# Kernel tuning notes

Hardware: AMD Instinct MI355X
Metric: run time of the kernel (lower is better)

The kernel has to match this reference:

```python
import jax, jax.numpy as jnp
import numpy as np

CONFIDENCE = 0.1
EPS = 1e-3  # keras BatchNormalization default epsilon
B, H, W, C = 4, 64, 64, 256


def setup_inputs() -> dict:
    key = jax.random.key(0)
    ks = jax.random.split(key, 6)
    return {
        "x": jax.random.normal(ks[0], (B, H, W, C), jnp.float32),
        "ca_gamma": jnp.ones((C,), jnp.float32),
        "ca_beta": jnp.zeros((C,), jnp.float32),
        "ca_mean": jnp.zeros((C,), jnp.float32),
        "ca_var": jnp.ones((C,), jnp.float32),
        "wq": jax.random.normal(ks[1], (C, C), jnp.float32) * 0.05,
        "wk": jax.random.normal(ks[2], (C, C), jnp.float32) * 0.05,
        "wv": jax.random.normal(ks[3], (C, C), jnp.float32) * 0.05,
        "wp": jax.random.normal(ks[4], (C, C), jnp.float32) * 0.05,
        "bn_gamma": jnp.ones((C,), jnp.float32),
        "bn_beta": jnp.zeros((C,), jnp.float32),
        "bn_mean": jnp.zeros((C,), jnp.float32),
        "bn_var": jnp.ones((C,), jnp.float32),
        "w_qkv": jax.random.normal(ks[5], (C, 3), jnp.float32) * 0.05,
    }


def _bn(x, g, b, m, v):
    # keras BatchNormalization, inference mode
    return (x - m) * jax.lax.rsqrt(v + EPS) * g + b


def reference(x, ca_gamma, ca_beta, ca_mean, ca_var, wq, wk, wv, wp,
              bn_gamma, bn_beta, bn_mean, bn_var, w_qkv):
    b, h, w, c = x.shape
    # ---- ChannelAttention (TRACER Channel_Tracer; dropout = identity at inference) ----
    gap = x.mean(axis=(1, 2))                         # [B, C] global average pool
    gn = _bn(gap, ca_gamma, ca_beta, ca_mean, ca_var)  # [B, C]
    q = gn @ wq                                        # 1x1 conv on 1x1 map == matmul
    k = gn @ wk
    v = gn @ wv
    logits = q[:, :, None] * k[:, None, :]             # [B, C, C], head_dim = 1
    score = jax.nn.softmax(logits, axis=-1)
    att = jnp.einsum('bij,bj->bi', score, v)           # [B, C]
    cmask = jax.nn.sigmoid(att @ wp)                   # [B, C] channel mask (alpha)
    ca_out = x * cmask[:, None, None, :] + x           # residual channel re-weighting
    # ---- UnionAttention spatial part ----
    co = _bn(ca_out, bn_gamma, bn_beta, bn_mean, bn_var)
    thr = jnp.percentile(cmask, CONFIDENCE * 100.0, axis=-1,
                         keepdims=True, method='linear')  # [B, 1]
    pmask = jnp.where(cmask > thr, cmask, 0.0)          # percentile masking
    co = co * pmask[:, None, None, :]
    qkv = jnp.einsum('bhwc,cf->bhwf', co, w_qkv)        # [B, H, W, 3] fused q/k/v 1x1 conv
    n = h * w
    qs = qkv[..., 0].reshape(b, n)                      # [B, N], head_dim = 1
    ks_ = qkv[..., 1].reshape(b, n)
    vs = qkv[..., 2].reshape(b, n)
    sl = qs[:, :, None] * ks_[:, None, :]               # [B, N, N] scores (outer product)
    sw = jax.nn.softmax(sl, axis=-1)
    sa = jnp.einsum('bij,bj->bi', sw, vs)               # [B, N]
    return qkv[..., 2:3] + sa.reshape(b, h, w, 1)       # v + attention, [B, H, W, 1]
```

## Files before the change

kernel.cpp:

```cpp
#include <hip/hip_runtime.h>

#define EPS 1e-3f

#define OFF_PGAP   0
#define OFF_PART   81920
#define OFF_AW     196608
#define OFF_BIAS   198656
#define OFF_QS     215040
#define OFF_KS     231424
#define OFF_VS     247808

#define L2E 1.4426950408889634f

__device__ __forceinline__ void st_wt2(float* p, float a, float b) {
    union { float f[2]; unsigned long long u; } x; x.f[0] = a; x.f[1] = b;
    __hip_atomic_store((unsigned long long*)p, x.u, __ATOMIC_RELAXED,
                       __HIP_MEMORY_SCOPE_AGENT);
}

__device__ unsigned g_done;

__global__ __launch_bounds__(512) void k_gap(
    const float* __restrict__ x,
    const float* __restrict__ wq, const float* __restrict__ wk,
    const float* __restrict__ wv, const float* __restrict__ wp,
    const float* __restrict__ bng, const float* __restrict__ bnb,
    const float* __restrict__ bnm, const float* __restrict__ bnv,
    const float* __restrict__ cag, const float* __restrict__ cab,
    const float* __restrict__ cam, const float* __restrict__ cav,
    float* __restrict__ pgap)
{
    __shared__ float4 s4[512];
    int blk = blockIdx.x;
    int t = threadIdx.x;
    int lane = t & 63, sub = t >> 6;

    if (t < 256) {
        const float* wmat = (blk < 64) ? wq : (blk < 128) ? wk
                          : (blk < 192) ? wv : wp;
        float4 w4 = *(const float4*)(wmat + (size_t)(blk & 63) * 1024 + 4 * t);
        asm volatile("" :: "v"(w4.x), "v"(w4.y), "v"(w4.z), "v"(w4.w));
    }
    if (blk == 1 && t < 256) {
        float z = bng[t] + bnb[t] + bnm[t] + bnv[t];
        asm volatile("" :: "v"(z));
    }
    if (blk == 2 && t < 256) {
        float z = cag[t] + cab[t] + cam[t] + cav[t];
        asm volatile("" :: "v"(z));
    }

    const float* xp = x + ((size_t)blk * 64 + sub * 8) * 256 + 4 * lane;
    float4 s = make_float4(0.f, 0.f, 0.f, 0.f);
    #pragma unroll
    for (int u = 0; u < 8; ++u) {
        float4 v = *(const float4*)(xp + (size_t)u * 256);
        s.x += v.x; s.y += v.y; s.z += v.z; s.w += v.w;
    }
    s4[sub * 64 + lane] = s;
    __syncthreads();
    if (t < 64) {
        float4 o = s4[t];
        #pragma unroll
        for (int p = 1; p < 8; ++p) {
            float4 v = s4[p * 64 + t];
            o.x += v.x; o.y += v.y; o.z += v.z; o.w += v.w;
        }
        *(float4*)(pgap + blk * 256 + 4 * t) = o;
    }
}

__global__ __launch_bounds__(512) void k_qkvmid(
    const float* __restrict__ pgap,
    const float* __restrict__ cag, const float* __restrict__ cab,
    const float* __restrict__ cam, const float* __restrict__ cav,
    const float* __restrict__ wq, const float* __restrict__ wk,
    const float* __restrict__ wv, const float* __restrict__ wp,
    const float* __restrict__ bng, const float* __restrict__ bnb,
    const float* __restrict__ bnm, const float* __restrict__ bnv,
    const float* __restrict__ wqkv,
    float* __restrict__ part, float* __restrict__ Aw, float* __restrict__ biasW)
{
    __shared__ float smem[4360];
    __shared__ int sBatch;
    int blk = blockIdx.x;
    int m = blk / 32, g = blk % 32;
    int r0 = g * 8;
    int t = threadIdx.x;
    int lane = t & 63, sub = t >> 6;
    const float* W = (m == 0) ? wq : (m == 1) ? wk : wv;

    {
        float* gpart = smem;
        float* gn_s  = smem + 512;
        float* red   = smem + 1536;
        {
            int b = t >> 7, row = (t >> 4) & 7, p4 = t & 15;
            float s = 0.f;
            #pragma unroll
            for (int q = 0; q < 4; ++q)
                s += pgap[(size_t)(b * 64 + p4 * 4 + q) * 256 + r0 + row];
            gpart[b * 128 + row * 16 + p4] = s;
        }
        __syncthreads();
        if (t < 32) {
            int b = t >> 3, row = t & 7;
            float s = 0.f;
            #pragma unroll
            for (int p = 0; p < 16; ++p) s += gpart[b * 128 + row * 16 + p];
            float gv = s * (1.0f / 4096.0f);
            int c = r0 + row;
            float sc = cag[c] * rsqrtf(cav[c] + EPS);
            gn_s[b * 8 + row] = gv * sc + (cab[c] - cam[c] * sc);
        }
        __syncthreads();
        {
            int c = t & 255, h = t >> 8;
            float a0 = 0.f, a1 = 0.f, a2 = 0.f, a3 = 0.f;
            #pragma unroll
            for (int rr = 0; rr < 4; ++rr) {
                int ri = h * 4 + rr;
                float w = W[(size_t)(r0 + ri) * 256 + c];
                a0 = fmaf(gn_s[0 * 8 + ri], w, a0);
                a1 = fmaf(gn_s[1 * 8 + ri], w, a1);
                a2 = fmaf(gn_s[2 * 8 + ri], w, a2);
                a3 = fmaf(gn_s[3 * 8 + ri], w, a3);
            }
            red[(h * 4 + 0) * 256 + c] = a0;
            red[(h * 4 + 1) * 256 + c] = a1;
            red[(h * 4 + 2) * 256 + c] = a2;
            red[(h * 4 + 3) * 256 + c] = a3;
        }
        __syncthreads();
        {
            int b = t >> 7, c0 = (t & 127) * 2;
            float v0 = red[b * 256 + c0]     + red[(4 + b) * 256 + c0];
            float v1 = red[b * 256 + c0 + 1] + red[(4 + b) * 256 + c0 + 1];
            st_wt2(part + (size_t)((m * 32 + g) * 4 + b) * 256 + c0, v0, v1);
        }
    }
    __syncthreads();
    if (t == 0) {
        unsigned v = __hip_atomic_fetch_add(&g_done, 1u, __ATOMIC_ACQ_REL,
                                            __HIP_MEMORY_SCOPE_AGENT);
        unsigned r = v % 96u;
        int batch = (int)r - 92;
        if (batch >= 0) {
            unsigned target = v - r + 96u;
            unsigned tries = 0;
            while (__hip_atomic_load(&g_done, __ATOMIC_RELAXED,
                                     __HIP_MEMORY_SCOPE_AGENT) < target) {
                __builtin_amdgcn_s_sleep(1);
                if (++tries > 8000000u) break;
            }
        }
        sBatch = batch;
    }
    __syncthreads();
    if (sBatch < 0) return;

    {
        int b = sBatch;
        float* sq  = smem;
        float* sk  = smem + 256;
        float* sv  = smem + 512;
        float* att = smem + 768;
        float* cmv = smem + 1024;
        float* Bc  = smem + 1280;
        float* red = smem + 1536;
        float* swq = smem + 3584;
        float* sc2 = smem + 4352;

        if (t < 384) { swq[t] = wqkv[t]; swq[t + 384] = wqkv[t + 384]; }

        if (t < 384) {
            int mm = t >> 7, c0 = (t & 127) * 2;
            float a0 = 0.f, a1 = 0.f;
            #pragma unroll 8
            for (int gg = 0; gg < 32; ++gg) {
                float2 v = *(const float2*)(part +
                              (size_t)((mm * 32 + gg) * 4 + b) * 256 + c0);
                a0 += v.x; a1 += v.y;
            }
            float* dst = (mm == 0) ? sq : (mm == 1) ? sk : sv;
            dst[c0] = a0; dst[c0 + 1] = a1;
        }
        __syncthreads();

        if (t < 64) {
            float mx = -1e30f, mn = 1e30f;
            #pragma unroll
            for (int u = 0; u < 4; ++u) {
                float v = sk[t + u * 64];
                mx = fmaxf(mx, v); mn = fminf(mn, v);
            }
            #pragma unroll
            for (int m2 = 1; m2 < 64; m2 <<= 1) {
                mx = fmaxf(mx, __shfl_xor(mx, m2, 64));
                mn = fminf(mn, __shfl_xor(mn, m2, 64));
            }
            if (t == 0) { sc2[0] = mx; sc2[1] = mn; }
        }
        __syncthreads();

        {
            int c = t & 255, h = t >> 8;
            float a = sq[c];
            float mrow = (a >= 0.f) ? a * sc2[0] : a * sc2[1];
            float a2 = a * L2E, m2 = mrow * L2E;
            const float* skp = sk + h * 128;
            const float* svp = sv + h * 128;
            float den = 0.f, num = 0.f;
            #pragma unroll 4
            for (int j = 0; j < 128; ++j) {
                float e = __builtin_amdgcn_exp2f(fmaf(a2, skp[j], -m2));
                den += e; num = fmaf(e, svp[j], num);
            }
            red[h * 256 + c] = den;
            red[512 + h * 256 + c] = num;
        }
        __syncthreads();
        if (t < 256)
            att[t] = (red[512 + t] + red[768 + t]) / (red[t] + red[256 + t]);
        __syncthreads();

        {
            int rg = sub, c4 = lane * 4;
            float4 ac = make_float4(0.f, 0.f, 0.f, 0.f);
            const float* wpp = wp + (size_t)rg * 32 * 256 + c4;
            #pragma unroll 8
            for (int i = 0; i < 32; ++i) {
                float gv = att[rg * 32 + i];
                float4 w = *(const float4*)(wpp + (size_t)i * 256);
                ac.x = fmaf(gv, w.x, ac.x); ac.y = fmaf(gv, w.y, ac.y);
                ac.z = fmaf(gv, w.z, ac.z); ac.w = fmaf(gv, w.w, ac.w);
            }
            *(float4*)(red + rg * 256 + c4) = ac;
        }
        __syncthreads();
        if (t < 256) {
            float ac = 0.f;
            #pragma unroll
            for (int r = 0; r < 8; ++r) ac += red[r * 256 + t];
            cmv[t] = 1.0f / (1.0f + __expf(-ac));
        }
        __syncthreads();

        if (t < 256) {
            float my = cmv[t];
            int rank = 0;
            for (int j = 0; j < 256; ++j) {
                float o = cmv[j];
                rank += (o < my) ? 1 : ((o == my && j < t) ? 1 : 0);
            }
            if (rank == 25) sc2[2] = my;
            if (rank == 26) sc2[3] = my;
        }
        __syncthreads();
        if (t == 0) sc2[4] = sc2[2] + 0.5f * (sc2[3] - sc2[2]);
        __syncthreads();

        if (t < 256) {
            float s2 = bng[t] * rsqrtf(bnv[t] + EPS);
            float o2 = bnb[t] - bnm[t] * s2;
            float cc = cmv[t];
            float pm = (cc > sc2[4]) ? cc : 0.f;
            Aw[b * 256 + t] = (1.f + cc) * s2 * pm;
            Bc[t] = o2 * pm;
        }
        __syncthreads();
        if (t < 3) {
            float s3 = 0.f;
            for (int ch = 0; ch < 256; ++ch)
                s3 = fmaf(Bc[ch], swq[ch * 3 + t], s3);
            biasW[b * 3 + t] = s3;
        }
    }
}

__global__ __launch_bounds__(256) void k_qkv(
    const float* __restrict__ x, const float* __restrict__ A,
    const float* __restrict__ wqkv, const float* __restrict__ bias,
    float* __restrict__ qs, float* __restrict__ ks, float* __restrict__ vs)
{
    int t = threadIdx.x;
    int lane = t & 63;
    int sl = lane & 31;
    int half = lane >> 5;
    int wid = (blockIdx.x * 256 + t) >> 6;
    union { float4 v4[6]; float f[24]; } W;
    #pragma unroll
    for (int i = 0; i < 6; ++i)
        W.v4[i] = *(const float4*)(wqkv + 24 * sl + 4 * i);
    #pragma unroll
    for (int b = 0; b < 4; ++b) {
        int pix = b * 4096 + wid * 2 + half;
        const float* xp = x + (size_t)pix * 256 + sl * 8;
        float4 xv0 = *(const float4*)(xp);
        float4 xv1 = *(const float4*)(xp + 4);
        float4 a0 = *(const float4*)(A + b * 256 + sl * 8);
        float4 a1 = *(const float4*)(A + b * 256 + sl * 8 + 4);
        float bq = bias[b * 3 + 0];
        float bk = bias[b * 3 + 1];
        float bv = bias[b * 3 + 2];
        float tt0 = xv0.x * a0.x, tt1 = xv0.y * a0.y;
        float tt2 = xv0.z * a0.z, tt3 = xv0.w * a0.w;
        float tt4 = xv1.x * a1.x, tt5 = xv1.y * a1.y;
        float tt6 = xv1.z * a1.z, tt7 = xv1.w * a1.w;
        float q = tt0 * W.f[0] + tt1 * W.f[3] + tt2 * W.f[6] + tt3 * W.f[9]
                + tt4 * W.f[12] + tt5 * W.f[15] + tt6 * W.f[18] + tt7 * W.f[21];
        float k = tt0 * W.f[1] + tt1 * W.f[4] + tt2 * W.f[7] + tt3 * W.f[10]
                + tt4 * W.f[13] + tt5 * W.f[16] + tt6 * W.f[19] + tt7 * W.f[22];
        float v = tt0 * W.f[2] + tt1 * W.f[5] + tt2 * W.f[8] + tt3 * W.f[11]
                + tt4 * W.f[14] + tt5 * W.f[17] + tt6 * W.f[20] + tt7 * W.f[23];
        #pragma unroll
        for (int m2 = 1; m2 < 32; m2 <<= 1) {
            q += __shfl_xor(q, m2, 64);
            k += __shfl_xor(k, m2, 64);
            v += __shfl_xor(v, m2, 64);
        }
        if (sl == 0) {
            qs[pix] = q + bq; ks[pix] = k + bk; vs[pix] = v + bv;
        }
    }
}

__global__ __launch_bounds__(512) void k_attn2(
    const float* __restrict__ qs, const float* __restrict__ ks,
    const float* __restrict__ vs, float* __restrict__ out)
{
    __shared__ float4 skv[2048];
    __shared__ float pden[8][64], pnum[8][64];
    __shared__ float rmax[8], rmin[8];
    int blk = blockIdx.x;
    int b = blk >> 6, ic = blk & 63;
    int t = threadIdx.x;
    int lane = t & 63, sub = t >> 6;
    int base = b * 4096;

    const float4* k4 = (const float4*)(ks + base);
    const float4* v4 = (const float4*)(vs + base);
    float kmx = -1e30f, kmn = 1e30f;
    #pragma unroll
    for (int u = 0; u < 2; ++u) {
        int i = t + u * 512;
        float4 kk = k4[i], vv = v4[i];
        skv[i * 2]     = make_float4(kk.x, vv.x, kk.y, vv.y);
        skv[i * 2 + 1] = make_float4(kk.z, vv.z, kk.w, vv.w);
        kmx = fmaxf(kmx, fmaxf(fmaxf(kk.x, kk.y), fmaxf(kk.z, kk.w)));
        kmn = fminf(kmn, fminf(fminf(kk.x, kk.y), fminf(kk.z, kk.w)));
    }
    #pragma unroll
    for (int m2 = 1; m2 < 64; m2 <<= 1) {
        kmx = fmaxf(kmx, __shfl_xor(kmx, m2, 64));
        kmn = fminf(kmn, __shfl_xor(kmn, m2, 64));
    }
    if (lane == 0) { rmax[sub] = kmx; rmin[sub] = kmn; }
    __syncthreads();
    float mx = rmax[0], mn = rmin[0];
    #pragma unroll
    for (int s = 1; s < 8; ++s) { mx = fmaxf(mx, rmax[s]); mn = fminf(mn, rmin[s]); }

    int row = ic * 64 + lane;
    float a = qs[base + row];
    float mrow = (a >= 0.f) ? a * mx : a * mn;
    float a2 = a * L2E, m2v = mrow * L2E;
    float den0 = 0.f, num0 = 0.f, den1 = 0.f, num1 = 0.f;
    const float4* sp = skv + sub * 256;
    #pragma unroll 4
    for (int j = 0; j < 256; ++j) {
        float4 kv = sp[j];
        float e0 = __builtin_amdgcn_exp2f(fmaf(a2, kv.x, -m2v));
        float e1 = __builtin_amdgcn_exp2f(fmaf(a2, kv.z, -m2v));
        den0 += e0; num0 = fmaf(e0, kv.y, num0);
        den1 += e1; num1 = fmaf(e1, kv.w, num1);
    }
    pden[sub][lane] = den0 + den1;
    pnum[sub][lane] = num0 + num1;
    __syncthreads();
    if (t < 64) {
        float den = 0.f, num = 0.f;
        #pragma unroll
        for (int s = 0; s < 8; ++s) { den += pden[s][t]; num += pnum[s][t]; }
        int r = ic * 64 + t;
        float vrow = (r & 1) ? skv[r >> 1].w : skv[r >> 1].y;
        out[base + r] = vrow + num / den;
    }
}

extern "C" void kernel_launch(void* const* d_in, const int* in_sizes, int n_in,
                              void* d_out, int out_size, void* d_ws, size_t ws_size,
                              hipStream_t stream) {
    const float* x    = (const float*)d_in[0];
    const float* cag  = (const float*)d_in[1];
    const float* cab  = (const float*)d_in[2];
    const float* cam  = (const float*)d_in[3];
    const float* cav  = (const float*)d_in[4];
    const float* wq   = (const float*)d_in[5];
    const float* wk   = (const float*)d_in[6];
    const float* wv   = (const float*)d_in[7];
    const float* wp   = (const float*)d_in[8];
    const float* bng  = (const float*)d_in[9];
    const float* bnb  = (const float*)d_in[10];
    const float* bnm  = (const float*)d_in[11];
    const float* bnv  = (const float*)d_in[12];
    const float* wqkv = (const float*)d_in[13];

    float* ws   = (float*)d_ws;
    float* pgap = ws + OFF_PGAP;
    float* part = ws + OFF_PART;
    float* Aw   = ws + OFF_AW;
    float* bias = ws + OFF_BIAS;
    float* qs   = ws + OFF_QS;
    float* ks   = ws + OFF_KS;
    float* vs   = ws + OFF_VS;

    k_gap<<<dim3(256), dim3(512), 0, stream>>>(x, wq, wk, wv, wp,
                                               bng, bnb, bnm, bnv,
                                               cag, cab, cam, cav, pgap);
    k_qkvmid<<<dim3(96), dim3(512), 0, stream>>>(pgap, cag, cab, cam, cav,
                                                 wq, wk, wv, wp,
                                                 bng, bnb, bnm, bnv, wqkv,
                                                 part, Aw, bias);
    k_qkv<<<dim3(512), dim3(256), 0, stream>>>(x, Aw, wqkv, bias, qs, ks, vs);
    k_attn2<<<dim3(256), dim3(512), 0, stream>>>(qs, ks, vs, (float*)d_out);
}
```

Baseline: 126.8 us.

## Fuse four kernels into two using device-wide atomic grid barriers

```diff
diff --git a/kernel.cpp b/kernel.cpp
--- a/kernel.cpp
+++ b/kernel.cpp
@@ -6,72 +6,26 @@
 #define OFF_PART   81920
 #define OFF_AW     196608
 #define OFF_BIAS   198656
-#define OFF_QS     215040
-#define OFF_KS     231424
+#define OFF_KS     215040
 #define OFF_VS     247808
 
 #define L2E 1.4426950408889634f
 
+__device__ __forceinline__ void st_wt(float* p, float v) {
+    __hip_atomic_store(p, v, __ATOMIC_RELAXED, __HIP_MEMORY_SCOPE_AGENT);
+}
 __device__ __forceinline__ void st_wt2(float* p, float a, float b) {
     union { float f[2]; unsigned long long u; } x; x.f[0] = a; x.f[1] = b;
     __hip_atomic_store((unsigned long long*)p, x.u, __ATOMIC_RELAXED,
                        __HIP_MEMORY_SCOPE_AGENT);
 }
 
+__device__ unsigned g_ctr1;
 __device__ unsigned g_done;
-
-__global__ __launch_bounds__(512) void k_gap(
+__device__ unsigned g_doneB[4 * 32];
+
+__global__ __launch_bounds__(512) void k_gapmid(
     const float* __restrict__ x,
-    const float* __restrict__ wq, const float* __restrict__ wk,
-    const float* __restrict__ wv, const float* __restrict__ wp,
-    const float* __restrict__ bng, const float* __restrict__ bnb,
-    const float* __restrict__ bnm, const float* __restrict__ bnv,
-    const float* __restrict__ cag, const float* __restrict__ cab,
-    const float* __restrict__ cam, const float* __restrict__ cav,
-    float* __restrict__ pgap)
-{
-    __shared__ float4 s4[512];
-    int blk = blockIdx.x;
-    int t = threadIdx.x;
-    int lane = t & 63, sub = t >> 6;
-
-    if (t < 256) {
-        const float* wmat = (blk < 64) ? wq : (blk < 128) ? wk
-                          : (blk < 192) ? wv : wp;
-        float4 w4 = *(const float4*)(wmat + (size_t)(blk & 63) * 1024 + 4 * t);
-        asm volatile("" :: "v"(w4.x), "v"(w4.y), "v"(w4.z), "v"(w4.w));
-    }
-    if (blk == 1 && t < 256) {
-        float z = bng[t] + bnb[t] + bnm[t] + bnv[t];
-        asm volatile("" :: "v"(z));
-    }
-    if (blk == 2 && t < 256) {
-        float z = cag[t] + cab[t] + cam[t] + cav[t];
-        asm volatile("" :: "v"(z));
-    }
-
-    const float* xp = x + ((size_t)blk * 64 + sub * 8) * 256 + 4 * lane;
-    float4 s = make_float4(0.f, 0.f, 0.f, 0.f);
-    #pragma unroll
-    for (int u = 0; u < 8; ++u) {
-        float4 v = *(const float4*)(xp + (size_t)u * 256);
-        s.x += v.x; s.y += v.y; s.z += v.z; s.w += v.w;
-    }
-    s4[sub * 64 + lane] = s;
-    __syncthreads();
-    if (t < 64) {
-        float4 o = s4[t];
-        #pragma unroll
-        for (int p = 1; p < 8; ++p) {
-            float4 v = s4[p * 64 + t];
-            o.x += v.x; o.y += v.y; o.z += v.z; o.w += v.w;
-        }
-        *(float4*)(pgap + blk * 256 + 4 * t) = o;
-    }
-}
-
-__global__ __launch_bounds__(512) void k_qkvmid(
-    const float* __restrict__ pgap,
     const float* __restrict__ cag, const float* __restrict__ cab,
     const float* __restrict__ cam, const float* __restrict__ cav,
     const float* __restrict__ wq, const float* __restrict__ wk,
@@ -79,17 +33,72 @@
     const float* __restrict__ bng, const float* __restrict__ bnb,
     const float* __restrict__ bnm, const float* __restrict__ bnv,
     const float* __restrict__ wqkv,
-    float* __restrict__ part, float* __restrict__ Aw, float* __restrict__ biasW)
+    float* __restrict__ pgap, float* __restrict__ part,
+    float* __restrict__ Aw, float* __restrict__ biasW)
 {
     __shared__ float smem[4360];
     __shared__ int sBatch;
     int blk = blockIdx.x;
+    int t = threadIdx.x;
+    int lane = t & 63, sub = t >> 6;
+
+    {
+        if (t < 256) {
+            const float* wmat = (blk < 64) ? wq : (blk < 128) ? wk
+                              : (blk < 192) ? wv : wp;
+            float4 w4 = *(const float4*)(wmat + (size_t)(blk & 63) * 1024 + 4 * t);
+            asm volatile("" :: "v"(w4.x), "v"(w4.y), "v"(w4.z), "v"(w4.w));
+        }
+        if (blk == 1 && t < 256) {
+            float z = bng[t] + bnb[t] + bnm[t] + bnv[t];
+            asm volatile("" :: "v"(z));
+        }
+        if (blk == 2 && t < 256) {
+            float z = cag[t] + cab[t] + cam[t] + cav[t];
+            asm volatile("" :: "v"(z));
+        }
+        float4* s4 = (float4*)smem;
+        const float* xp = x + ((size_t)blk * 64 + sub * 8) * 256 + 4 * lane;
+        float4 s = make_float4(0.f, 0.f, 0.f, 0.f);
+        #pragma unroll
+        for (int u = 0; u < 8; ++u) {
+            float4 v = *(const float4*)(xp + (size_t)u * 256);
+            s.x += v.x; s.y += v.y; s.z += v.z; s.w += v.w;
+        }
+        s4[sub * 64 + lane] = s;
+        __syncthreads();
+        if (t < 64) {
+            float4 o = s4[t];
+            #pragma unroll
+            for (int p = 1; p < 8; ++p) {
+                float4 v = s4[p * 64 + t];
+                o.x += v.x; o.y += v.y; o.z += v.z; o.w += v.w;
+            }
+            st_wt2(pgap + blk * 256 + 4 * t,     o.x, o.y);
+            st_wt2(pgap + blk * 256 + 4 * t + 2, o.z, o.w);
+        }
+    }
+    __syncthreads();
+
+    if (t == 0) {
+        unsigned v = __hip_atomic_fetch_add(&g_ctr1, 1u, __ATOMIC_ACQ_REL,
+                                            __HIP_MEMORY_SCOPE_AGENT);
+        if (blk < 96) {
+            unsigned target = v - (v % 256u) + 256u;
+            unsigned tries = 0;
+            while (__hip_atomic_load(&g_ctr1, __ATOMIC_RELAXED,
+                                     __HIP_MEMORY_SCOPE_AGENT) < target) {
+                __builtin_amdgcn_s_sleep(1);
+                if (++tries > 8000000u) break;
+            }
+        }
+    }
+    __syncthreads();
+    if (blk >= 96) return;
+
     int m = blk / 32, g = blk % 32;
     int r0 = g * 8;
-    int t = threadIdx.x;
-    int lane = t & 63, sub = t >> 6;
     const float* W = (m == 0) ? wq : (m == 1) ? wk : wv;
-
     {
         float* gpart = smem;
         float* gn_s  = smem + 512;
@@ -278,113 +287,125 @@
     }
 }
 
-__global__ __launch_bounds__(256) void k_qkv(
-    const float* __restrict__ x, const float* __restrict__ A,
-    const float* __restrict__ wqkv, const float* __restrict__ bias,
-    float* __restrict__ qs, float* __restrict__ ks, float* __restrict__ vs)
-{
-    int t = threadIdx.x;
-    int lane = t & 63;
-    int sl = lane & 31;
-    int half = lane >> 5;
-    int wid = (blockIdx.x * 256 + t) >> 6;
-    union { float4 v4[6]; float f[24]; } W;
-    #pragma unroll
-    for (int i = 0; i < 6; ++i)
-        W.v4[i] = *(const float4*)(wqkv + 24 * sl + 4 * i);
-    #pragma unroll
-    for (int b = 0; b < 4; ++b) {
-        int pix = b * 4096 + wid * 2 + half;
-        const float* xp = x + (size_t)pix * 256 + sl * 8;
-        float4 xv0 = *(const float4*)(xp);
-        float4 xv1 = *(const float4*)(xp + 4);
-        float4 a0 = *(const float4*)(A + b * 256 + sl * 8);
-        float4 a1 = *(const float4*)(A + b * 256 + sl * 8 + 4);
-        float bq = bias[b * 3 + 0];
-        float bk = bias[b * 3 + 1];
-        float bv = bias[b * 3 + 2];
-        float tt0 = xv0.x * a0.x, tt1 = xv0.y * a0.y;
-        float tt2 = xv0.z * a0.z, tt3 = xv0.w * a0.w;
-        float tt4 = xv1.x * a1.x, tt5 = xv1.y * a1.y;
-        float tt6 = xv1.z * a1.z, tt7 = xv1.w * a1.w;
-        float q = tt0 * W.f[0] + tt1 * W.f[3] + tt2 * W.f[6] + tt3 * W.f[9]
-                + tt4 * W.f[12] + tt5 * W.f[15] + tt6 * W.f[18] + tt7 * W.f[21];
-        float k = tt0 * W.f[1] + tt1 * W.f[4] + tt2 * W.f[7] + tt3 * W.f[10]
-                + tt4 * W.f[13] + tt5 * W.f[16] + tt6 * W.f[19] + tt7 * W.f[22];
-        float v = tt0 * W.f[2] + tt1 * W.f[5] + tt2 * W.f[8] + tt3 * W.f[11]
-                + tt4 * W.f[14] + tt5 * W.f[17] + tt6 * W.f[20] + tt7 * W.f[23];
-        #pragma unroll
-        for (int m2 = 1; m2 < 32; m2 <<= 1) {
-            q += __shfl_xor(q, m2, 64);
-            k += __shfl_xor(k, m2, 64);
-            v += __shfl_xor(v, m2, 64);
-        }
-        if (sl == 0) {
-            qs[pix] = q + bq; ks[pix] = k + bk; vs[pix] = v + bv;
-        }
-    }
-}
-
-__global__ __launch_bounds__(512) void k_attn2(
-    const float* __restrict__ qs, const float* __restrict__ ks,
-    const float* __restrict__ vs, float* __restrict__ out)
+__global__ __launch_bounds__(512) void k_qkvattn(
+    const float* __restrict__ x, const float* __restrict__ Aw,
+    const float* __restrict__ wqkv, const float* __restrict__ biasW,
+    float* __restrict__ ks, float* __restrict__ vs, float* __restrict__ out)
 {
     __shared__ float4 skv[2048];
     __shared__ float pden[8][64], pnum[8][64];
     __shared__ float rmax[8], rmin[8];
+    __shared__ float qown[64];
     int blk = blockIdx.x;
     int b = blk >> 6, ic = blk & 63;
     int t = threadIdx.x;
     int lane = t & 63, sub = t >> 6;
+    int sl = lane & 31, half = lane >> 5;
     int base = b * 4096;
 
-    const float4* k4 = (const float4*)(ks + base);
-    const float4* v4 = (const float4*)(vs + base);
-    float kmx = -1e30f, kmn = 1e30f;
-    #pragma unroll
-    for (int u = 0; u < 2; ++u) {
-        int i = t + u * 512;
-        float4 kk = k4[i], vv = v4[i];
-        skv[i * 2]     = make_float4(kk.x, vv.x, kk.y, vv.y);
-        skv[i * 2 + 1] = make_float4(kk.z, vv.z, kk.w, vv.w);
-        kmx = fmaxf(kmx, fmaxf(fmaxf(kk.x, kk.y), fmaxf(kk.z, kk.w)));
-        kmn = fminf(kmn, fminf(fminf(kk.x, kk.y), fminf(kk.z, kk.w)));
-    }
-    #pragma unroll
-    for (int m2 = 1; m2 < 64; m2 <<= 1) {
-        kmx = fmaxf(kmx, __shfl_xor(kmx, m2, 64));
-        kmn = fminf(kmn, __shfl_xor(kmn, m2, 64));
-    }
-    if (lane == 0) { rmax[sub] = kmx; rmin[sub] = kmn; }
-    __syncthreads();
-    float mx = rmax[0], mn = rmin[0];
-    #pragma unroll
-    for (int s = 1; s < 8; ++s) { mx = fmaxf(mx, rmax[s]); mn = fminf(mn, rmin[s]); }
-
-    int row = ic * 64 + lane;
-    float a = qs[base + row];
-    float mrow = (a >= 0.f) ? a * mx : a * mn;
-    float a2 = a * L2E, m2v = mrow * L2E;
-    float den0 = 0.f, num0 = 0.f, den1 = 0.f, num1 = 0.f;
-    const float4* sp = skv + sub * 256;
-    #pragma unroll 4
-    for (int j = 0; j < 256; ++j) {
-        float4 kv = sp[j];
-        float e0 = __builtin_amdgcn_exp2f(fmaf(a2, kv.x, -m2v));
-        float e1 = __builtin_amdgcn_exp2f(fmaf(a2, kv.z, -m2v));
-        den0 += e0; num0 = fmaf(e0, kv.y, num0);
-        den1 += e1; num1 = fmaf(e1, kv.w, num1);
-    }
-    pden[sub][lane] = den0 + den1;
-    pnum[sub][lane] = num0 + num1;
-    __syncthreads();
-    if (t < 64) {
-        float den = 0.f, num = 0.f;
-        #pragma unroll
-        for (int s = 0; s < 8; ++s) { den += pden[s][t]; num += pnum[s][t]; }
-        int r = ic * 64 + t;
-        float vrow = (r & 1) ? skv[r >> 1].w : skv[r >> 1].y;
-        out[base + r] = vrow + num / den;
+    {
+        union { float4 v4[6]; float f[24]; } W;
+        #pragma unroll
+        for (int i = 0; i < 6; ++i)
+            W.v4[i] = *(const float4*)(wqkv + 24 * sl + 4 * i);
+        float4 a0 = *(const float4*)(Aw + b * 256 + sl * 8);
+        float4 a1 = *(const float4*)(Aw + b * 256 + sl * 8 + 4);
+        float bq = biasW[b * 3 + 0];
+        float bk = biasW[b * 3 + 1];
+        float bv = biasW[b * 3 + 2];
+        #pragma unroll
+        for (int it = 0; it < 4; ++it) {
+            int local = sub * 8 + it * 2 + half;
+            int pix = base + ic * 64 + local;
+            const float* xp = x + (size_t)pix * 256 + sl * 8;
+            float4 xv0 = *(const float4*)(xp);
+            float4 xv1 = *(const float4*)(xp + 4);
+            float tt0 = xv0.x * a0.x, tt1 = xv0.y * a0.y;
+            float tt2 = xv0.z * a0.z, tt3 = xv0.w * a0.w;
+            float tt4 = xv1.x * a1.x, tt5 = xv1.y * a1.y;
+            float tt6 = xv1.z * a1.z, tt7 = xv1.w * a1.w;
+            float q = tt0 * W.f[0] + tt1 * W.f[3] + tt2 * W.f[6] + tt3 * W.f[9]
+                    + tt4 * W.f[12] + tt5 * W.f[15] + tt6 * W.f[18] + tt7 * W.f[21];
+            float k = tt0 * W.f[1] + tt1 * W.f[4] + tt2 * W.f[7] + tt3 * W.f[10]
+                    + tt4 * W.f[13] + tt5 * W.f[16] + tt6 * W.f[19] + tt7 * W.f[22];
+            float v = tt0 * W.f[2] + tt1 * W.f[5] + tt2 * W.f[8] + tt3 * W.f[11]
+                    + tt4 * W.f[14] + tt5 * W.f[17] + tt6 * W.f[20] + tt7 * W.f[23];
+            #pragma unroll
+            for (int m2 = 1; m2 < 32; m2 <<= 1) {
+                q += __shfl_xor(q, m2, 64);
+                k += __shfl_xor(k, m2, 64);
+                v += __shfl_xor(v, m2, 64);
+            }
+            if (sl == 0) {
+                qown[local] = q + bq;
+                st_wt(ks + pix, k + bk);
+                st_wt(vs + pix, v + bv);
+            }
+        }
+    }
+    __syncthreads();
+    if (t == 0) {
+        unsigned v = __hip_atomic_fetch_add(&g_doneB[b * 32], 1u,
+                                            __ATOMIC_ACQ_REL,
+                                            __HIP_MEMORY_SCOPE_AGENT);
+        unsigned target = v - (v % 64u) + 64u;
+        unsigned tries = 0;
+        while (__hip_atomic_load(&g_doneB[b * 32], __ATOMIC_RELAXED,
+                                 __HIP_MEMORY_SCOPE_AGENT) < target) {
+            __builtin_amdgcn_s_sleep(1);
+            if (++tries > 8000000u) break;
+        }
+    }
+    __syncthreads();
+
+    {
+        const float4* k4 = (const float4*)(ks + base);
+        const float4* v4 = (const float4*)(vs + base);
+        float kmx = -1e30f, kmn = 1e30f;
+        #pragma unroll
+        for (int u = 0; u < 2; ++u) {
+            int i = t + u * 512;
+            float4 kk = k4[i], vv = v4[i];
+            skv[i * 2]     = make_float4(kk.x, vv.x, kk.y, vv.y);
+            skv[i * 2 + 1] = make_float4(kk.z, vv.z, kk.w, vv.w);
+            kmx = fmaxf(kmx, fmaxf(fmaxf(kk.x, kk.y), fmaxf(kk.z, kk.w)));
+            kmn = fminf(kmn, fminf(fminf(kk.x, kk.y), fminf(kk.z, kk.w)));
+        }
+        #pragma unroll
+        for (int m2 = 1; m2 < 64; m2 <<= 1) {
+            kmx = fmaxf(kmx, __shfl_xor(kmx, m2, 64));
+            kmn = fminf(kmn, __shfl_xor(kmn, m2, 64));
+        }
+        if (lane == 0) { rmax[sub] = kmx; rmin[sub] = kmn; }
+        __syncthreads();
+        float mx = rmax[0], mn = rmin[0];
+        #pragma unroll
+        for (int s = 1; s < 8; ++s) { mx = fmaxf(mx, rmax[s]); mn = fminf(mn, rmin[s]); }
+
+        float a = qown[lane];
+        float mrow = (a >= 0.f) ? a * mx : a * mn;
+        float a2 = a * L2E, m2v = mrow * L2E;
+        float den0 = 0.f, num0 = 0.f, den1 = 0.f, num1 = 0.f;
+        const float4* sp = skv + sub * 256;
+        #pragma unroll 4
+        for (int j = 0; j < 256; ++j) {
+            float4 kv = sp[j];
+            float e0 = __builtin_amdgcn_exp2f(fmaf(a2, kv.x, -m2v));
+            float e1 = __builtin_amdgcn_exp2f(fmaf(a2, kv.z, -m2v));
+            den0 += e0; num0 = fmaf(e0, kv.y, num0);
+            den1 += e1; num1 = fmaf(e1, kv.w, num1);
+        }
+        pden[sub][lane] = den0 + den1;
+        pnum[sub][lane] = num0 + num1;
+        __syncthreads();
+        if (t < 64) {
+            float den = 0.f, num = 0.f;
+            #pragma unroll
+            for (int s = 0; s < 8; ++s) { den += pden[s][t]; num += pnum[s][t]; }
+            int r = ic * 64 + t;
+            float vrow = (r & 1) ? skv[r >> 1].w : skv[r >> 1].y;
+            out[base + r] = vrow + num / den;
+        }
     }
 }
 
@@ -411,17 +432,13 @@
     float* part = ws + OFF_PART;
     float* Aw   = ws + OFF_AW;
     float* bias = ws + OFF_BIAS;
-    float* qs   = ws + OFF_QS;
     float* ks   = ws + OFF_KS;
     float* vs   = ws + OFF_VS;
 
-    k_gap<<<dim3(256), dim3(512), 0, stream>>>(x, wq, wk, wv, wp,
-                                               bng, bnb, bnm, bnv,
-                                               cag, cab, cam, cav, pgap);
-    k_qkvmid<<<dim3(96), dim3(512), 0, stream>>>(pgap, cag, cab, cam, cav,
-                                                 wq, wk, wv, wp,
-                                                 bng, bnb, bnm, bnv, wqkv,
-                                                 part, Aw, bias);
-    k_qkv<<<dim3(512), dim3(256), 0, stream>>>(x, Aw, wqkv, bias, qs, ks, vs);
-    k_attn2<<<dim3(256), dim3(512), 0, stream>>>(qs, ks, vs, (float*)d_out);
+    k_gapmid<<<dim3(256), dim3(512), 0, stream>>>(x, cag, cab, cam, cav,
+                                                  wq, wk, wv, wp,
+                                                  bng, bnb, bnm, bnv, wqkv,
+                                                  pgap, part, Aw, bias);
+    k_qkvattn<<<dim3(256), dim3(512), 0, stream>>>(x, Aw, wqkv, bias,
+                                                   ks, vs, (float*)d_out);
 }
```

New measurement: 137.7 us. +8.6%, slower.
